# Performance work log

Hardware: AMD Instinct MI355X
Metric: run time of the kernel (lower is better)

The kernel has to match this reference:

```python
import jax, jax.numpy as jnp
import numpy as np

B, N, D_MODEL = 16, 65536, 512
NBUCKETS = 11
BN_EPS = 1e-5
LN_EPS = 1e-5


def setup_inputs() -> dict:
    key = jax.random.key(0)
    ks = jax.random.split(key, 12)
    def w(k, shape, fan_in):
        return jax.random.normal(k, shape, jnp.float32) * (1.0 / np.sqrt(fan_in))
    return {
        "x": jax.random.normal(ks[0], (B, N, 3), jnp.float32),
        "w1": w(ks[1], (3, 64), 3),   "b1": jnp.zeros((64,), jnp.float32),
        "g1": jnp.ones((64,), jnp.float32),  "be1": jnp.zeros((64,), jnp.float32),
        "w2": w(ks[2], (64, 128), 64), "b2": jnp.zeros((128,), jnp.float32),
        "g2": jnp.ones((128,), jnp.float32), "be2": jnp.zeros((128,), jnp.float32),
        "w3": w(ks[3], (128, 256), 128), "b3": jnp.zeros((256,), jnp.float32),
        "g3": jnp.ones((256,), jnp.float32), "be3": jnp.zeros((256,), jnp.float32),
        "wp": w(ks[4], (518, D_MODEL), 518), "bp": jnp.zeros((D_MODEL,), jnp.float32),
        "g_ln": jnp.ones((D_MODEL,), jnp.float32), "b_ln": jnp.zeros((D_MODEL,), jnp.float32),
    }


def _bn(h, g, b):
    # BatchNorm1d in training mode: biased variance over the flattened batch axis
    m = jnp.mean(h, axis=0)
    v = jnp.mean((h - m) ** 2, axis=0)
    return (h - m) * jax.lax.rsqrt(v + BN_EPS) * g + b


def reference(x, w1, b1, g1, be1, w2, b2, g2, be2, w3, b3, g3, be3, wp, bp, g_ln, b_ln):
    Bb, Nn, _ = x.shape
    x_flat = x.reshape(Bb * Nn, 3)
    h = jax.nn.relu(_bn(x_flat @ w1 + b1, g1, be1))
    h = jax.nn.relu(_bn(h @ w2 + b2, g2, be2))
    h = jax.nn.relu(_bn(h @ w3 + b3, g3, be3))
    feat = h.reshape(Bb, Nn, 256)

    # y-bucket histogram means of (x, z) coordinates, vectorized via segment_sum
    y = x[:, :, 1]
    y_min = jnp.min(y, axis=1, keepdims=True)
    y_max = jnp.max(y, axis=1, keepdims=True)
    y_norm = (y - y_min) / (y_max - y_min + 1e-6)
    buckets = jnp.clip((y_norm * 10).astype(jnp.int32), 0, NBUCKETS - 1)  # (B,N) in [0,10]
    seg = (jnp.arange(Bb, dtype=jnp.int32)[:, None] * NBUCKETS + buckets).reshape(-1)
    nseg = Bb * NBUCKETS
    sx = jax.ops.segment_sum(x[:, :, 0].reshape(-1), seg, num_segments=nseg)
    sz = jax.ops.segment_sum(x[:, :, 2].reshape(-1), seg, num_segments=nseg)
    cnt = jax.ops.segment_sum(jnp.ones((Bb * Nn,), jnp.float32), seg, num_segments=nseg)
    denom = jnp.maximum(cnt, 1.0)
    cx = (sx / denom).reshape(Bb, NBUCKETS)
    cz = (sz / denom).reshape(Bb, NBUCKETS)
    x_centers = jnp.take_along_axis(cx, buckets, axis=1)  # (B,N)
    z_centers = jnp.take_along_axis(cz, buckets, axis=1)

    dx = x[:, :, 0] - x_centers
    dz = x[:, :, 2] - z_centers
    theta = jnp.arctan2(dz, dx)
    r = jnp.sqrt(dx ** 2 + dz ** 2)
    spatial = jnp.stack([jnp.sin(theta), jnp.cos(theta), r], axis=-1)  # (B,N,3)

    feat = jnp.concatenate([feat, spatial], axis=-1)  # (B,N,259)
    feat_max = jnp.max(feat, axis=1)
    feat_avg = jnp.mean(feat, axis=1)
    feat_cat = jnp.concatenate([feat_max, feat_avg], axis=1)  # (B,518)

    out = feat_cat @ wp + bp
    mu = jnp.mean(out, axis=-1, keepdims=True)
    var = jnp.mean((out - mu) ** 2, axis=-1, keepdims=True)
    return (out - mu) * jax.lax.rsqrt(var + LN_EPS) * g_ln + b_ln
```

## Files before the change

### kernel.cpp

```cpp
#include <hip/hip_runtime.h>
#include <stdint.h>

#define B_    16
#define N_    65536
#define NPTS  (B_*N_)
#define NBK   11
#define NFEAT 259
#define NF    ((float)NPTS)

typedef float f32x4 __attribute__((ext_vector_type(4)));
typedef short s16x8 __attribute__((ext_vector_type(8)));
union frag_u { s16x8 v; unsigned u[4]; };
union x24_u  { float4 v4[6]; float f[24]; };

enum {
  OFF_YMINF = 16,
  OFF_YMAXF = 32,
  OFF_A1    = 64,
  OFF_C1    = 128,
  OFF_A2    = 192,
  OFF_C2    = 320,
  OFF_CX    = 448,
  OFF_CZ    = 624,
  OFF_A3    = 800,
  OFF_C3    = 1056,
  OFF_GC    = 2048,
  OFF_G1S   = 6144,
  OFF_H3C   = 6400,
  OFF_PSTR  = 16384,
  OFF_PBKT  = 24576,
  OFF_PSPA  = 43008,
  OFF_PG    = 49152,
  OFF_PGS   = 2146304,
  OFF_PH3   = 2179072,
  OFF_PPOOL = 2703360
};

__device__ __forceinline__ float wave_sum(float v){
  #pragma unroll
  for (int m=32;m>=1;m>>=1) v += __shfl_xor(v,m,64);
  return v;
}
__device__ __forceinline__ float wave_max(float v){
  #pragma unroll
  for (int m=32;m>=1;m>>=1) v = fmaxf(v,__shfl_xor(v,m,64));
  return v;
}
__device__ __forceinline__ float wave_min(float v){
  #pragma unroll
  for (int m=32;m>=1;m>>=1) v = fminf(v,__shfl_xor(v,m,64));
  return v;
}
__device__ __forceinline__ unsigned short bf16_bits(float f){
  unsigned u=__float_as_uint(f);
  u += 0x7FFFu + ((u>>16)&1u);
  return (unsigned short)(u>>16);
}
__device__ __forceinline__ unsigned cvt_pk_bf16(float lo, float hi){
  unsigned r;
  asm("v_cvt_pk_bf16_f32 %0, %1, %2" : "=v"(r) : "v"(lo), "v"(hi));
  return r;
}

__global__ __launch_bounds__(256) void k_stream0(const float* __restrict__ x,
                                                 float* __restrict__ ws){
  __shared__ float red[4][12];
  const int t=threadIdx.x, l=t&63, w=t>>6;
  const int bid=blockIdx.x;
  const float4* xv=(const float4*)(x + (size_t)bid*2048*3);
  float s0=0,s1=0,s2=0,q00=0,q01=0,q02=0,q11=0,q12=0,q22=0;
  float ymn=3.4e38f, ymx=-3.4e38f;
  #pragma unroll
  for (int i=0;i<2;i++){
    const int vi=(i*256+t)*3;
    const float4 a=xv[vi], b4=xv[vi+1], c=xv[vi+2];
    float X[4]={a.x,a.w,b4.z,c.y};
    float Y[4]={a.y,b4.x,b4.w,c.z};
    float Z[4]={a.z,b4.y,c.x,c.w};
    #pragma unroll
    for (int p=0;p<4;p++){
      s0+=X[p]; s1+=Y[p]; s2+=Z[p];
      q00=fmaf(X[p],X[p],q00); q01=fmaf(X[p],Y[p],q01); q02=fmaf(X[p],Z[p],q02);
      q11=fmaf(Y[p],Y[p],q11); q12=fmaf(Y[p],Z[p],q12); q22=fmaf(Z[p],Z[p],q22);
      ymn=fminf(ymn,Y[p]); ymx=fmaxf(ymx,Y[p]);
    }
  }
  s0=wave_sum(s0); s1=wave_sum(s1); s2=wave_sum(s2);
  q00=wave_sum(q00); q01=wave_sum(q01); q02=wave_sum(q02);
  q11=wave_sum(q11); q12=wave_sum(q12); q22=wave_sum(q22);
  ymn=wave_min(ymn); ymx=wave_max(ymx);
  if (l==0){
    red[w][0]=s0; red[w][1]=s1; red[w][2]=s2;
    red[w][3]=q00; red[w][4]=q01; red[w][5]=q02;
    red[w][6]=q11; red[w][7]=q12; red[w][8]=q22;
    red[w][9]=ymn; red[w][10]=ymx;
  }
  __syncthreads();
  if (t<11){
    const float v0=red[0][t],v1=red[1][t],v2=red[2][t],v3=red[3][t];
    float r;
    if (t==9)       r=fminf(fminf(v0,v1),fminf(v2,v3));
    else if (t==10) r=fmaxf(fmaxf(v0,v1),fmaxf(v2,v3));
    else            r=v0+v1+v2+v3;
    ws[OFF_PSTR+bid*16+t]=r;
  }
}

__global__ void k_finA(const float* __restrict__ w1, const float* __restrict__ b1,
                       const float* __restrict__ gm, const float* __restrict__ bt,
                       float* __restrict__ ws){
  __shared__ float sums[9];
  const int t=threadIdx.x;
  if (t<9){
    float s=0.f;
    #pragma unroll 8
    for (int blk=0;blk<512;blk++) s+=ws[OFF_PSTR+blk*16+t];
    sums[t]=s;
  }
  if (t>=32&&t<48){
    const int b=t-32; float m=3.4e38f;
    #pragma unroll 8
    for (int blk=0;blk<32;blk++) m=fminf(m,ws[OFF_PSTR+(b*32+blk)*16+9]);
    ws[OFF_YMINF+b]=m;
  }
  if (t>=48&&t<64){
    const int b=t-48; float m=-3.4e38f;
    #pragma unroll 8
    for (int blk=0;blk<32;blk++) m=fmaxf(m,ws[OFF_PSTR+(b*32+blk)*16+10]);
    ws[OFF_YMAXF+b]=m;
  }
  __syncthreads();
  if (t<64){
    const float i_n=1.f/NF;
    const float w0=w1[t], wa=w1[64+t], wb=w1[128+t];
    const float ms=(w0*sums[0]+wa*sums[1]+wb*sums[2])*i_n;
    const float es=(w0*w0*sums[3]+wa*wa*sums[6]+wb*wb*sums[8]
                   +2.f*(w0*wa*sums[4]+w0*wb*sums[5]+wa*wb*sums[7]))*i_n;
    const float var=es-ms*ms;
    const float a=gm[t]/sqrtf(var+1e-5f);
    ws[OFF_A1+t]=a; ws[OFF_C1+t]=bt[t]-(ms+b1[t])*a;
  }
}

__global__ __launch_bounds__(256) void k_bucket(const float* __restrict__ x,
                                                float* __restrict__ ws){
  __shared__ float red[4][12];
  const int t=threadIdx.x, l=t&63, w=t>>6;
  const int bid=blockIdx.x, b=bid>>5;
  const float ymn=ws[OFF_YMINF+b], ymx=ws[OFF_YMAXF+b];
  const float4* xv=(const float4*)(x + (size_t)bid*2048*3);
  float sxl[NBK], szl[NBK], cntl[NBK];
  #pragma unroll
  for (int k=0;k<NBK;k++){ sxl[k]=0.f; szl[k]=0.f; cntl[k]=0.f; }
  #pragma unroll
  for (int i=0;i<2;i++){
    const int vi=(i*256+t)*3;
    const float4 a=xv[vi], b4=xv[vi+1], c=xv[vi+2];
    float X[4]={a.x,a.w,b4.z,c.y};
    float Y[4]={a.y,b4.x,b4.w,c.z};
    float Z[4]={a.z,b4.y,c.x,c.w};
    #pragma unroll
    for (int p=0;p<4;p++){
      const float yn=(Y[p]-ymn)/(ymx-ymn+1e-6f);
      int bk=(int)(yn*10.f); bk = bk<0?0:(bk>10?10:bk);
      #pragma unroll
      for (int k=0;k<NBK;k++){
        const bool m=(bk==k);
        sxl[k]+= m?X[p]:0.f; szl[k]+= m?Z[p]:0.f; cntl[k]+= m?1.f:0.f;
      }
    }
  }
  #pragma unroll
  for (int k=0;k<NBK;k++){
    const float s=wave_sum(sxl[k]);
    if (l==0) red[w][k]=s;
  }
  __syncthreads();
  if (t<NBK) ws[OFF_PBKT+bid*36+t]=red[0][t]+red[1][t]+red[2][t]+red[3][t];
  __syncthreads();
  #pragma unroll
  for (int k=0;k<NBK;k++){
    const float z=wave_sum(szl[k]);
    if (l==0) red[w][k]=z;
  }
  __syncthreads();
  if (t<NBK) ws[OFF_PBKT+bid*36+11+t]=red[0][t]+red[1][t]+red[2][t]+red[3][t];
  __syncthreads();
  #pragma unroll
  for (int k=0;k<NBK;k++){
    const float c=wave_sum(cntl[k]);
    if (l==0) red[w][k]=c;
  }
  __syncthreads();
  if (t<NBK) ws[OFF_PBKT+bid*36+22+t]=red[0][t]+red[1][t]+red[2][t]+red[3][t];
}

__global__ __launch_bounds__(256) void k_spatial(const float* __restrict__ x,
                                                 float* __restrict__ ws){
  __shared__ float red[4][8];
  const int t=threadIdx.x, l=t&63, w=t>>6;
  const int bid=blockIdx.x, b=bid>>5;
  const float ymn=ws[OFF_YMINF+b], ymx=ws[OFF_YMAXF+b];
  const float4* xv=(const float4*)(x + (size_t)bid*2048*3);
  float mx[3]={-3.4e38f,-3.4e38f,-3.4e38f}, sm[3]={0.f,0.f,0.f};
  #pragma unroll
  for (int i=0;i<2;i++){
    const int vi=(i*256+t)*3;
    const float4 a=xv[vi], b4=xv[vi+1], c=xv[vi+2];
    float X[4]={a.x,a.w,b4.z,c.y};
    float Y[4]={a.y,b4.x,b4.w,c.z};
    float Z[4]={a.z,b4.y,c.x,c.w};
    #pragma unroll
    for (int p=0;p<4;p++){
      const float yn=(Y[p]-ymn)/(ymx-ymn+1e-6f);
      int bk=(int)(yn*10.f); bk = bk<0?0:(bk>10?10:bk);
      const float dx=X[p]-ws[OFF_CX+b*NBK+bk];
      const float dz=Z[p]-ws[OFF_CZ+b*NBK+bk];
      const float r=sqrtf(fmaf(dx,dx,dz*dz));
      const float sn=(r>0.f)?(dz/r):0.f;
      const float cs=(r>0.f)?(dx/r):1.f;
      mx[0]=fmaxf(mx[0],sn); sm[0]+=sn;
      mx[1]=fmaxf(mx[1],cs); sm[1]+=cs;
      mx[2]=fmaxf(mx[2],r);  sm[2]+=r;
    }
  }
  #pragma unroll
  for (int q=0;q<3;q++){
    const float m=wave_max(mx[q]);
    const float s=wave_sum(sm[q]);
    if (l==0){ red[w][q]=m; red[w][4+q]=s; }
  }
  __syncthreads();
  if (t<3)        ws[OFF_PSPA+bid*8+t]  =fmaxf(fmaxf(red[0][t],red[1][t]),fmaxf(red[2][t],red[3][t]));
  else if (t>=4&&t<7){
    const int q=t-4;
    ws[OFF_PSPA+bid*8+4+q]=red[0][4+q]+red[1][4+q]+red[2][4+q]+red[3][4+q];
  }
}

__global__ __launch_bounds__(512,2) void k_gram(
    const float* __restrict__ x,
    const float* __restrict__ w1, const float* __restrict__ b1,
    float* __restrict__ ws)
{
  const int t=threadIdx.x, w=t>>6, l=t&63, lg=l>>4, lr=l&15;
  const int bid=blockIdx.x;
  const int ti=w>>1, tj0=(w&1)*2, tj1=tj0+1;
  const float* A1=ws+OFF_A1; const float* C1=ws+OFF_C1;
  float wA[4], wB0[4], wB1[4];
  {
    const int fA=16*ti+lr;  const float aA=A1[fA];
    wA[0]=w1[fA]*aA;  wA[1]=w1[64+fA]*aA;  wA[2]=w1[128+fA]*aA;  wA[3]=b1[fA]*aA+C1[fA];
    const int f0=16*tj0+lr; const float a0=A1[f0];
    wB0[0]=w1[f0]*a0; wB0[1]=w1[64+f0]*a0; wB0[2]=w1[128+f0]*a0; wB0[3]=b1[f0]*a0+C1[f0];
    const int f1=16*tj1+lr; const float a1=A1[f1];
    wB1[0]=w1[f1]*a1; wB1[1]=w1[64+f1]*a1; wB1[2]=w1[128+f1]*a1; wB1[3]=b1[f1]*a1+C1[f1];
  }
  f32x4 acc0={0.f,0.f,0.f,0.f}, acc1={0.f,0.f,0.f,0.f};
  float s1=0.f;
  const float* xb = x + (size_t)bid*2048*3;
  #pragma unroll 1
  for (int step=0; step<64; ++step){
    x24_u xa;
    const float4* xp=(const float4*)(xb + (step*32+8*lg)*3);
    #pragma unroll
    for (int i=0;i<6;i++) xa.v4[i]=xp[i];
    float gA[8],gB0[8],gB1[8];
    #pragma unroll
    for (int j=0;j<8;j++){
      const float X=xa.f[3*j], Y=xa.f[3*j+1], Z=xa.f[3*j+2];
      gA[j] =fmaxf(fmaf(X,wA[0], fmaf(Y,wA[1], fmaf(Z,wA[2], wA[3]))),0.f);
      gB0[j]=fmaxf(fmaf(X,wB0[0],fmaf(Y,wB0[1],fmaf(Z,wB0[2],wB0[3]))),0.f);
      gB1[j]=fmaxf(fmaf(X,wB1[0],fmaf(Y,wB1[1],fmaf(Z,wB1[2],wB1[3]))),0.f);
    }
    frag_u fA,f0,f1;
    #pragma unroll
    for (int m=0;m<4;m++){
      fA.u[m]=cvt_pk_bf16(gA[2*m],gA[2*m+1]);
      f0.u[m]=cvt_pk_bf16(gB0[2*m],gB0[2*m+1]);
      f1.u[m]=cvt_pk_bf16(gB1[2*m],gB1[2*m+1]);
    }
    acc0=__builtin_amdgcn_mfma_f32_16x16x32_bf16(fA.v,f0.v,acc0,0,0,0);
    acc1=__builtin_amdgcn_mfma_f32_16x16x32_bf16(fA.v,f1.v,acc1,0,0,0);
    if (!(w&1)){
      #pragma unroll
      for (int j=0;j<8;j++) s1+=gA[j];
    }
  }
  #pragma unroll
  for (int q=0;q<4;q++){
    ws[OFF_PG + (size_t)((16*ti+4*lg+q)*64 + 16*tj0+lr)*512 + bid]=acc0[q];
    ws[OFF_PG + (size_t)((16*ti+4*lg+q)*64 + 16*tj1+lr)*512 + bid]=acc1[q];
  }
  if (!(w&1)){
    s1+=__shfl_xor(s1,16); s1+=__shfl_xor(s1,32);
    if (l<16) ws[OFF_PGS + (16*ti+lr)*512 + bid]=s1;
  }
}

__global__ __launch_bounds__(256) void k_redG(float* __restrict__ ws){
  __shared__ float red[256];
  const int t=threadIdx.x, blk=blockIdx.x;
  if (blk<64){
    const int e=blk*64+(t>>2), q=t&3;
    float s=0.f;
    const float* p=ws+OFF_PG+(size_t)e*512+q*128;
    #pragma unroll 8
    for (int i=0;i<128;i++) s+=p[i];
    red[t]=s; __syncthreads();
    if (q==0) ws[OFF_GC+e]=red[t]+red[t+1]+red[t+2]+red[t+3];
  } else {
    const int f=t>>2, q=t&3;
    float s=0.f;
    const float* p=ws+OFF_PGS+(size_t)f*512+q*128;
    #pragma unroll 8
    for (int i=0;i<128;i++) s+=p[i];
    red[t]=s; __syncthreads();
    if (q==0) ws[OFF_G1S+f]=red[t]+red[t+1]+red[t+2]+red[t+3];
  }
}

__global__ __launch_bounds__(256) void k_finB2(
    const float* __restrict__ w2, const float* __restrict__ b2,
    const float* __restrict__ gm, const float* __restrict__ bt,
    float* __restrict__ ws){
  __shared__ float red[256];
  __shared__ float red2[64];
  const int t=threadIdx.x, j=blockIdx.x;
  if (j<128){
    float acc=0.f;
    #pragma unroll
    for (int p=0;p<16;p++){
      const int idx=p*256+t;
      const int r=idx>>6, c=idx&63;
      acc += w2[r*128+j]*ws[OFF_GC+r*64+c]*w2[c*128+j];
    }
    red[t]=acc;
    if (t<64) red2[t]=w2[t*128+j]*ws[OFF_G1S+t];
    __syncthreads();
    for (int s=128;s>0;s>>=1){ if (t<s) red[t]+=red[t+s]; __syncthreads(); }
    if (t<32) red2[t]+=red2[t+32];
    __syncthreads();
    if (t==0){
      float sw=0.f;
      #pragma unroll
      for (int i=0;i<32;i++) sw+=red2[i];
      const float i_n=1.f/NF;
      const float bj=b2[j];
      const float m=sw*i_n+bj;
      const float e2=(red[0]+2.f*bj*sw)*i_n+bj*bj;
      const float var=e2-m*m;
      const float a=gm[j]/sqrtf(var+1e-5f);
      ws[OFF_A2+j]=a; ws[OFF_C2+j]=bt[j]-m*a;
    }
  } else {
    if (t<176){
      const int b=t/NBK, k=t-b*NBK;
      float sx=0.f, sz=0.f, cn=0.f;
      #pragma unroll 8
      for (int blk=0;blk<32;blk++){
        const int p=OFF_PBKT+(b*32+blk)*36;
        sx+=ws[p+k]; sz+=ws[p+11+k]; cn+=ws[p+22+k];
      }
      const float d=fmaxf(cn,1.f);
      ws[OFF_CX+t]=sx/d; ws[OFF_CZ+t]=sz/d;
    }
  }
}

template<int MODE>
__global__ __launch_bounds__(512) void k_mlp(
    const float* __restrict__ x,
    const float* __restrict__ w1, const float* __restrict__ b1,
    const float* __restrict__ w2, const float* __restrict__ b2,
    const float* __restrict__ w3, const float* __restrict__ b3,
    float* __restrict__ ws)
{
  __shared__ float xs[2048*3];
  __shared__ short g2t[2*128*136];
  const int t=threadIdx.x, w=t>>6, l=t&63, lg=l>>4, lr=l&15;
  const int bid=blockIdx.x;
  const int ptg=w&1, fgrp=w>>1;
  char* g2base=(char*)g2t;

  {
    const float4* xp=(const float4*)(x + (size_t)bid*2048*3);
    float4* xd=(float4*)xs;
    #pragma unroll
    for (int i=0;i<3;i++) xd[i*512+t]=xp[i*512+t];
  }

  const float* A1=ws+OFF_A1; const float* C1=ws+OFF_C1;
  float w1f[2][3][8], b1f[2][8];
  #pragma unroll
  for (int kt=0;kt<2;kt++)
    #pragma unroll
    for (int i=0;i<8;i++){
      const int f=kt*32+8*lg+i; const float a=A1[f];
      w1f[kt][0][i]=w1[f]*a; w1f[kt][1][i]=w1[64+f]*a; w1f[kt][2][i]=w1[128+f]*a;
      b1f[kt][i]=b1[f]*a+C1[f];
    }

  s16x8 w2f[2][2]; float b2i[2][4];
  #pragma unroll
  for (int j=0;j<2;j++){
    const int col2=(2*fgrp+j)*16+lr;
    const float sc2=ws[OFF_A2+col2];
    #pragma unroll
    for (int kt=0;kt<2;kt++)
      #pragma unroll
      for (int i=0;i<8;i++)
        w2f[j][kt][i]=(short)bf16_bits(w2[(kt*32+8*lg+i)*128+col2]*sc2);
    #pragma unroll
    for (int r=0;r<4;r++){
      const int f2=(2*fgrp+j)*16+4*lg+r;
      b2i[j][r]=ws[OFF_A2+f2]*b2[f2]+ws[OFF_C2+f2];
    }
  }

  s16x8 w3f[4][4]; float b3i[4][4];
  #pragma unroll
  for (int j=0;j<4;j++){
    const int col3=(4*fgrp+j)*16+lr;
    const float sc3=(MODE==1)?1.f:ws[OFF_A3+col3];
    #pragma unroll
    for (int kt=0;kt<4;kt++)
      #pragma unroll
      for (int i=0;i<8;i++)
        w3f[j][kt][i]=(short)bf16_bits(w3[(kt*32+8*lg+i)*256+col3]*sc3);
    #pragma unroll
    for (int r=0;r<4;r++){
      const int f3=(4*fgrp+j)*16+4*lg+r;
      b3i[j][r]=(MODE==1)? b3[f3] : (ws[OFF_A3+f3]*b3[f3]+ws[OFF_C3+f3]);
    }
  }

  float aS[4][4], aQ[4][4];
  #pragma unroll
  for (int j=0;j<4;j++)
    #pragma unroll
    for (int r=0;r<4;r++){ aS[j][r]=(MODE==2)?-3.4e38f:0.f; aQ[j][r]=0.f; }

  __syncthreads();

  int cur=0;
  #pragma unroll 1
  for (int it=0; it<16; ++it){
    char* g2cur=g2base + cur*(128*272);
    #pragma unroll
    for (int pt=0;pt<4;pt++){
      const int row=ptg*64+pt*16+lr;
      const int pidx=it*128+row;
      const float x0=xs[pidx*3+0], x1v=xs[pidx*3+1], x2=xs[pidx*3+2];
      frag_u bf[2];
      #pragma unroll
      for (int kt=0;kt<2;kt++){
        float h[8];
        #pragma unroll
        for (int i=0;i<8;i++){
          float v=b1f[kt][i];
          v=fmaf(x0,w1f[kt][0][i],v); v=fmaf(x1v,w1f[kt][1][i],v); v=fmaf(x2,w1f[kt][2][i],v);
          h[i]=fmaxf(v,0.f);
        }
        #pragma unroll
        for (int m=0;m<4;m++) bf[kt].u[m]=cvt_pk_bf16(h[2*m],h[2*m+1]);
      }
      #pragma unroll
      for (int j=0;j<2;j++){
        f32x4 acc={b2i[j][0],b2i[j][1],b2i[j][2],b2i[j][3]};
        acc=__builtin_amdgcn_mfma_f32_16x16x32_bf16(w2f[j][0],bf[0].v,acc,0,0,0);
        acc=__builtin_amdgcn_mfma_f32_16x16x32_bf16(w2f[j][1],bf[1].v,acc,0,0,0);
        const unsigned lo=cvt_pk_bf16(fmaxf(acc[0],0.f),fmaxf(acc[1],0.f));
        const unsigned hi=cvt_pk_bf16(fmaxf(acc[2],0.f),fmaxf(acc[3],0.f));
        *(uint2*)(g2cur + row*272 + fgrp*64 + j*32 + lg*8)=make_uint2(lo,hi);
      }
    }
    __syncthreads();
    #pragma unroll 1
    for (int pt=0;pt<4;pt++){
      const int row=ptg*64+pt*16+lr;
      const char* rp=g2cur + row*272;
      s16x8 bfr0=*(const s16x8*)(rp + lg*16);
      s16x8 bfr1=*(const s16x8*)(rp + 64 + lg*16);
      s16x8 bfr2=*(const s16x8*)(rp + 128 + lg*16);
      s16x8 bfr3=*(const s16x8*)(rp + 192 + lg*16);
      #pragma unroll
      for (int j=0;j<4;j++){
        f32x4 a3={b3i[j][0],b3i[j][1],b3i[j][2],b3i[j][3]};
        a3=__builtin_amdgcn_mfma_f32_16x16x32_bf16(w3f[j][0],bfr0,a3,0,0,0);
        a3=__builtin_amdgcn_mfma_f32_16x16x32_bf16(w3f[j][1],bfr1,a3,0,0,0);
        a3=__builtin_amdgcn_mfma_f32_16x16x32_bf16(w3f[j][2],bfr2,a3,0,0,0);
        a3=__builtin_amdgcn_mfma_f32_16x16x32_bf16(w3f[j][3],bfr3,a3,0,0,0);
        #pragma unroll
        for (int r=0;r<4;r++){
          if (MODE==1){
            const float h=a3[r]; aS[j][r]+=h; aQ[j][r]=fmaf(h,h,aQ[j][r]);
          } else {
            const float g=fmaxf(a3[r],0.f);
            aS[j][r]=fmaxf(aS[j][r],g); aQ[j][r]+=g;
          }
        }
      }
    }
    cur^=1;
  }

  const int slot=bid*2+ptg;
  #pragma unroll
  for (int j=0;j<4;j++)
    #pragma unroll
    for (int r=0;r<4;r++){
      const int f3=(4*fgrp+j)*16+4*lg+r;
      if (MODE==1){
        float s=aS[j][r], q=aQ[j][r];
        #pragma unroll
        for (int m=1;m<16;m<<=1){ s+=__shfl_xor(s,m); q+=__shfl_xor(q,m); }
        if (lr==0){
          ws[OFF_PH3 + (size_t)f3*1024 + slot]=s;
          ws[OFF_PH3 + (size_t)(256+f3)*1024 + slot]=q;
        }
      } else {
        float mxv=aS[j][r], s=aQ[j][r];
        #pragma unroll
        for (int m=1;m<16;m<<=1){ mxv=fmaxf(mxv,__shfl_xor(mxv,m)); s+=__shfl_xor(s,m); }
        if (lr==0){
          const int b=bid>>5, chunk=bid&31;
          ws[OFF_PPOOL + (size_t)b*512*64 + (size_t)f3*64 + chunk*2+ptg]=mxv;
          ws[OFF_PPOOL + (size_t)b*512*64 + (size_t)(256+f3)*64 + chunk*2+ptg]=s;
        }
      }
    }
}

__global__ __launch_bounds__(256) void k_redH3(float* __restrict__ ws){
  __shared__ float red[256];
  const int t=threadIdx.x, blk=blockIdx.x;
  const int col=blk*16+(t>>4), part=t&15;
  float s=0.f;
  const float* p=ws+OFF_PH3+(size_t)col*1024+part*64;
  #pragma unroll 8
  for (int i=0;i<64;i++) s+=p[i];
  red[t]=s; __syncthreads();
  if (part==0){
    float r=0.f;
    #pragma unroll
    for (int i=0;i<16;i++) r+=red[(t&~15)+i];
    ws[OFF_H3C+col]=r;
  }
}

__global__ void k_finC(const float* __restrict__ gm, const float* __restrict__ bt,
                       float* __restrict__ ws){
  const int t=threadIdx.x;
  if (t<256){
    const float i_n=1.f/NF;
    const float m=ws[OFF_H3C+t]*i_n;
    const float v=ws[OFF_H3C+256+t]*i_n-m*m;
    const float a=gm[t]/sqrtf(v+1e-5f);
    ws[OFF_A3+t]=a; ws[OFF_C3+t]=bt[t]-m*a;
  }
}

__global__ __launch_bounds__(256) void k_final(
    const float* __restrict__ wp, const float* __restrict__ bp,
    const float* __restrict__ gln, const float* __restrict__ bln,
    float* __restrict__ out, const float* __restrict__ ws)
{
  __shared__ float feat[518];
  __shared__ float red[256];
  const int b=blockIdx.x, t=threadIdx.x;
  {
    float fm=-3.4e38f, fs=0.f;
    const float* pm=ws+OFF_PPOOL+(size_t)b*512*64+(size_t)t*64;
    const float* psu=ws+OFF_PPOOL+(size_t)b*512*64+(size_t)(256+t)*64;
    #pragma unroll 8
    for (int s=0;s<64;s++){ fm=fmaxf(fm,pm[s]); fs+=psu[s]; }
    feat[t]=fm; feat[NFEAT+t]=fs*(1.f/65536.f);
  }
  if (t<3){
    float fm=-3.4e38f, fs=0.f;
    #pragma unroll 4
    for (int blk=0;blk<32;blk++){
      const int p=OFF_PSPA+(b*32+blk)*8;
      fm=fmaxf(fm,ws[p+t]);
      fs+=ws[p+4+t];
    }
    feat[256+t]=fm; feat[NFEAT+256+t]=fs*(1.f/65536.f);
  }
  __syncthreads();
  float o0=bp[t], o1=bp[t+256];
  #pragma unroll 4
  for (int i=0;i<518;i++){
    const float f=feat[i];
    o0=fmaf(f, wp[i*512+t],     o0);
    o1=fmaf(f, wp[i*512+t+256], o1);
  }
  red[t]=o0+o1; __syncthreads();
  for (int s=128;s>0;s>>=1){ if (t<s) red[t]+=red[t+s]; __syncthreads(); }
  const float mu=red[0]*(1.f/512.f);
  __syncthreads();
  const float d0=o0-mu, d1=o1-mu;
  red[t]=d0*d0+d1*d1; __syncthreads();
  for (int s=128;s>0;s>>=1){ if (t<s) red[t]+=red[t+s]; __syncthreads(); }
  const float var=red[0]*(1.f/512.f);
  const float rs=1.f/sqrtf(var+1e-5f);
  out[b*512+t]     = d0*rs*gln[t]    +bln[t];
  out[b*512+t+256] = d1*rs*gln[t+256]+bln[t+256];
}

extern "C" void kernel_launch(void* const* d_in, const int* in_sizes, int n_in,
                              void* d_out, int out_size, void* d_ws, size_t ws_size,
                              hipStream_t stream)
{
  const float* x  =(const float*)d_in[0];
  const float* w1 =(const float*)d_in[1];
  const float* b1 =(const float*)d_in[2];
  const float* gm1=(const float*)d_in[3];
  const float* be1=(const float*)d_in[4];
  const float* w2 =(const float*)d_in[5];
  const float* b2 =(const float*)d_in[6];
  const float* gm2=(const float*)d_in[7];
  const float* be2=(const float*)d_in[8];
  const float* w3 =(const float*)d_in[9];
  const float* b3 =(const float*)d_in[10];
  const float* gm3=(const float*)d_in[11];
  const float* be3=(const float*)d_in[12];
  const float* wp =(const float*)d_in[13];
  const float* bp =(const float*)d_in[14];
  const float* gln=(const float*)d_in[15];
  const float* bln=(const float*)d_in[16];
  float* ws=(float*)d_ws;
  float* out=(float*)d_out;

  k_stream0<<<dim3(512),dim3(256),0,stream>>>(x,ws);
  k_finA   <<<dim3(1),  dim3(256),0,stream>>>(w1,b1,gm1,be1,ws);
  k_bucket <<<dim3(512),dim3(256),0,stream>>>(x,ws);
  k_gram   <<<dim3(512),dim3(512),0,stream>>>(x,w1,b1,ws);
  k_redG   <<<dim3(65), dim3(256),0,stream>>>(ws);
  k_finB2  <<<dim3(129),dim3(256),0,stream>>>(w2,b2,gm2,be2,ws);
  k_spatial<<<dim3(512),dim3(256),0,stream>>>(x,ws);
  k_mlp<1> <<<dim3(512),dim3(512),0,stream>>>(x,w1,b1,w2,b2,w3,b3,ws);
  k_redH3  <<<dim3(32), dim3(256),0,stream>>>(ws);
  k_finC   <<<dim3(1),  dim3(256),0,stream>>>(gm3,be3,ws);
  k_mlp<2> <<<dim3(512),dim3(512),0,stream>>>(x,w1,b1,w2,b2,w3,b3,ws);
  k_final  <<<dim3(16), dim3(256),0,stream>>>(wp,bp,gln,bln,out,ws);
}
```

Measured before the change: 477.1 us.

## Restructure MLP kernel for two blocks per CU with shared layer-1 tile

```diff
diff --git a/kernel.cpp b/kernel.cpp
--- a/kernel.cpp
+++ b/kernel.cpp
@@ -33,7 +33,7 @@
   OFF_PG    = 49152,
   OFF_PGS   = 2146304,
   OFF_PH3   = 2179072,
-  OFF_PPOOL = 2703360
+  OFF_PPOOL = 3227648
 };
 
 __device__ __forceinline__ float wave_sum(float v){
@@ -369,39 +369,32 @@
 }
 
 template<int MODE>
-__global__ __launch_bounds__(512) void k_mlp(
+__global__ __launch_bounds__(512,2) void k_mlp(
     const float* __restrict__ x,
     const float* __restrict__ w1, const float* __restrict__ b1,
     const float* __restrict__ w2, const float* __restrict__ b2,
     const float* __restrict__ w3, const float* __restrict__ b3,
     float* __restrict__ ws)
 {
-  __shared__ float xs[2048*3];
-  __shared__ short g2t[2*128*136];
+  __shared__ short g1t[128*72];
+  __shared__ short g2t[128*136];
   const int t=threadIdx.x, w=t>>6, l=t&63, lg=l>>4, lr=l&15;
-  const int bid=blockIdx.x;
+  const int bid=blockIdx.x, b=bid>>6, chunk=bid&63;
   const int ptg=w&1, fgrp=w>>1;
-  char* g2base=(char*)g2t;
-
-  {
-    const float4* xp=(const float4*)(x + (size_t)bid*2048*3);
-    float4* xd=(float4*)xs;
-    #pragma unroll
-    for (int i=0;i<3;i++) xd[i*512+t]=xp[i*512+t];
-  }
-
-  const float* A1=ws+OFF_A1; const float* C1=ws+OFF_C1;
-  float w1f[2][3][8], b1f[2][8];
-  #pragma unroll
-  for (int kt=0;kt<2;kt++)
-    #pragma unroll
-    for (int i=0;i<8;i++){
-      const int f=kt*32+8*lg+i; const float a=A1[f];
-      w1f[kt][0][i]=w1[f]*a; w1f[kt][1][i]=w1[64+f]*a; w1f[kt][2][i]=w1[128+f]*a;
-      b1f[kt][i]=b1[f]*a+C1[f];
-    }
-
-  s16x8 w2f[2][2]; float b2i[2][4];
+  char* g1c=(char*)g1t; char* g2c=(char*)g2t;
+
+  const int fg=l&7, pj=(l>>3)&7;
+  const float* a1=ws+OFF_A1; const float* c1=ws+OFF_C1;
+  float w1f[3][8], b1f[8];
+  #pragma unroll
+  for (int i=0;i<8;i++){
+    const int f=8*fg+i; const float a=a1[f];
+    #pragma unroll
+    for (int q=0;q<3;q++) w1f[q][i]=w1[q*64+f]*a;
+    b1f[i]=b1[f]*a+c1[f];
+  }
+
+  s16x8 w2f[2][2]; float b2v[2][4];
   #pragma unroll
   for (int j=0;j<2;j++){
     const int col2=(2*fgrp+j)*16+lr;
@@ -414,11 +407,11 @@
     #pragma unroll
     for (int r=0;r<4;r++){
       const int f2=(2*fgrp+j)*16+4*lg+r;
-      b2i[j][r]=ws[OFF_A2+f2]*b2[f2]+ws[OFF_C2+f2];
-    }
-  }
-
-  s16x8 w3f[4][4]; float b3i[4][4];
+      b2v[j][r]=ws[OFF_A2+f2]*b2[f2]+ws[OFF_C2+f2];
+    }
+  }
+
+  s16x8 w3f[4][4]; float b3v[4][4];
   #pragma unroll
   for (int j=0;j<4;j++){
     const int col3=(4*fgrp+j)*16+lr;
@@ -431,7 +424,7 @@
     #pragma unroll
     for (int r=0;r<4;r++){
       const int f3=(4*fgrp+j)*16+4*lg+r;
-      b3i[j][r]=(MODE==1)? b3[f3] : (ws[OFF_A3+f3]*b3[f3]+ws[OFF_C3+f3]);
+      b3v[j][r]=(MODE==1)? b3[f3] : (ws[OFF_A3+f3]*b3[f3]+ws[OFF_C3+f3]);
     }
   }
 
@@ -441,56 +434,68 @@
     #pragma unroll
     for (int r=0;r<4;r++){ aS[j][r]=(MODE==2)?-3.4e38f:0.f; aQ[j][r]=0.f; }
 
-  __syncthreads();
-
-  int cur=0;
+  const int base=b*N_+chunk*1024;
+  const int ptl=16*w+2*pj;
+
+  float c0[3], c1v[3], n0[3], n1[3];
+  {
+    const float* xp=&x[(size_t)(base+ptl)*3];
+    #pragma unroll
+    for (int q=0;q<3;q++){ c0[q]=xp[q]; c1v[q]=xp[3+q]; }
+  }
+
   #pragma unroll 1
-  for (int it=0; it<16; ++it){
-    char* g2cur=g2base + cur*(128*272);
+  for (int it=0; it<8; ++it){
+    #pragma unroll
+    for (int s=0;s<2;s++){
+      const float x0=s?c1v[0]:c0[0], x1v=s?c1v[1]:c0[1], x2=s?c1v[2]:c0[2];
+      unsigned pk[4];
+      #pragma unroll
+      for (int i=0;i<4;i++){
+        float v0=b1f[2*i], v1=b1f[2*i+1];
+        v0=fmaf(x0,w1f[0][2*i],v0);  v1=fmaf(x0,w1f[0][2*i+1],v1);
+        v0=fmaf(x1v,w1f[1][2*i],v0); v1=fmaf(x1v,w1f[1][2*i+1],v1);
+        v0=fmaf(x2,w1f[2][2*i],v0);  v1=fmaf(x2,w1f[2][2*i+1],v1);
+        pk[i]=cvt_pk_bf16(fmaxf(v0,0.f),fmaxf(v1,0.f));
+      }
+      *(int4*)(g1c + (ptl+s)*144 + fg*16) = make_int4(pk[0],pk[1],pk[2],pk[3]);
+    }
+    if (it<7){
+      const float* xp=&x[(size_t)(base+(it+1)*128+ptl)*3];
+      #pragma unroll
+      for (int q=0;q<3;q++){ n0[q]=xp[q]; n1[q]=xp[3+q]; }
+    }
+    __syncthreads();
     #pragma unroll
     for (int pt=0;pt<4;pt++){
       const int row=ptg*64+pt*16+lr;
-      const int pidx=it*128+row;
-      const float x0=xs[pidx*3+0], x1v=xs[pidx*3+1], x2=xs[pidx*3+2];
-      frag_u bf[2];
-      #pragma unroll
-      for (int kt=0;kt<2;kt++){
-        float h[8];
-        #pragma unroll
-        for (int i=0;i<8;i++){
-          float v=b1f[kt][i];
-          v=fmaf(x0,w1f[kt][0][i],v); v=fmaf(x1v,w1f[kt][1][i],v); v=fmaf(x2,w1f[kt][2][i],v);
-          h[i]=fmaxf(v,0.f);
-        }
-        #pragma unroll
-        for (int m=0;m<4;m++) bf[kt].u[m]=cvt_pk_bf16(h[2*m],h[2*m+1]);
-      }
+      const s16x8 bf0=*(const s16x8*)(g1c + row*144 + lg*16);
+      const s16x8 bf1=*(const s16x8*)(g1c + row*144 + 64 + lg*16);
       #pragma unroll
       for (int j=0;j<2;j++){
-        f32x4 acc={b2i[j][0],b2i[j][1],b2i[j][2],b2i[j][3]};
-        acc=__builtin_amdgcn_mfma_f32_16x16x32_bf16(w2f[j][0],bf[0].v,acc,0,0,0);
-        acc=__builtin_amdgcn_mfma_f32_16x16x32_bf16(w2f[j][1],bf[1].v,acc,0,0,0);
+        f32x4 acc={b2v[j][0],b2v[j][1],b2v[j][2],b2v[j][3]};
+        acc=__builtin_amdgcn_mfma_f32_16x16x32_bf16(w2f[j][0],bf0,acc,0,0,0);
+        acc=__builtin_amdgcn_mfma_f32_16x16x32_bf16(w2f[j][1],bf1,acc,0,0,0);
         const unsigned lo=cvt_pk_bf16(fmaxf(acc[0],0.f),fmaxf(acc[1],0.f));
         const unsigned hi=cvt_pk_bf16(fmaxf(acc[2],0.f),fmaxf(acc[3],0.f));
-        *(uint2*)(g2cur + row*272 + fgrp*64 + j*32 + lg*8)=make_uint2(lo,hi);
+        *(uint2*)(g2c + row*272 + fgrp*64 + j*32 + lg*8) = make_uint2(lo,hi);
       }
     }
     __syncthreads();
     #pragma unroll 1
     for (int pt=0;pt<4;pt++){
       const int row=ptg*64+pt*16+lr;
-      const char* rp=g2cur + row*272;
-      s16x8 bfr0=*(const s16x8*)(rp + lg*16);
-      s16x8 bfr1=*(const s16x8*)(rp + 64 + lg*16);
-      s16x8 bfr2=*(const s16x8*)(rp + 128 + lg*16);
-      s16x8 bfr3=*(const s16x8*)(rp + 192 + lg*16);
+      const s16x8 bf0=*(const s16x8*)(g2c + row*272 + lg*16);
+      const s16x8 bf1=*(const s16x8*)(g2c + row*272 + 64 + lg*16);
+      const s16x8 bf2=*(const s16x8*)(g2c + row*272 + 128 + lg*16);
+      const s16x8 bf3=*(const s16x8*)(g2c + row*272 + 192 + lg*16);
       #pragma unroll
       for (int j=0;j<4;j++){
-        f32x4 a3={b3i[j][0],b3i[j][1],b3i[j][2],b3i[j][3]};
-        a3=__builtin_amdgcn_mfma_f32_16x16x32_bf16(w3f[j][0],bfr0,a3,0,0,0);
-        a3=__builtin_amdgcn_mfma_f32_16x16x32_bf16(w3f[j][1],bfr1,a3,0,0,0);
-        a3=__builtin_amdgcn_mfma_f32_16x16x32_bf16(w3f[j][2],bfr2,a3,0,0,0);
-        a3=__builtin_amdgcn_mfma_f32_16x16x32_bf16(w3f[j][3],bfr3,a3,0,0,0);
+        f32x4 a3={b3v[j][0],b3v[j][1],b3v[j][2],b3v[j][3]};
+        a3=__builtin_amdgcn_mfma_f32_16x16x32_bf16(w3f[j][0],bf0,a3,0,0,0);
+        a3=__builtin_amdgcn_mfma_f32_16x16x32_bf16(w3f[j][1],bf1,a3,0,0,0);
+        a3=__builtin_amdgcn_mfma_f32_16x16x32_bf16(w3f[j][2],bf2,a3,0,0,0);
+        a3=__builtin_amdgcn_mfma_f32_16x16x32_bf16(w3f[j][3],bf3,a3,0,0,0);
         #pragma unroll
         for (int r=0;r<4;r++){
           if (MODE==1){
@@ -502,10 +507,10 @@
         }
       }
     }
-    cur^=1;
-  }
-
-  const int slot=bid*2+ptg;
+    #pragma unroll
+    for (int q=0;q<3;q++){ c0[q]=n0[q]; c1v[q]=n1[q]; }
+  }
+
   #pragma unroll
   for (int j=0;j<4;j++)
     #pragma unroll
@@ -516,17 +521,18 @@
         #pragma unroll
         for (int m=1;m<16;m<<=1){ s+=__shfl_xor(s,m); q+=__shfl_xor(q,m); }
         if (lr==0){
-          ws[OFF_PH3 + (size_t)f3*1024 + slot]=s;
-          ws[OFF_PH3 + (size_t)(256+f3)*1024 + slot]=q;
+          const int slot=bid*2+ptg;
+          ws[OFF_PH3 + (size_t)f3*2048 + slot]=s;
+          ws[OFF_PH3 + (size_t)(256+f3)*2048 + slot]=q;
         }
       } else {
         float mxv=aS[j][r], s=aQ[j][r];
         #pragma unroll
         for (int m=1;m<16;m<<=1){ mxv=fmaxf(mxv,__shfl_xor(mxv,m)); s+=__shfl_xor(s,m); }
         if (lr==0){
-          const int b=bid>>5, chunk=bid&31;
-          ws[OFF_PPOOL + (size_t)b*512*64 + (size_t)f3*64 + chunk*2+ptg]=mxv;
-          ws[OFF_PPOOL + (size_t)b*512*64 + (size_t)(256+f3)*64 + chunk*2+ptg]=s;
+          const int slot=chunk*2+ptg;
+          ws[OFF_PPOOL + (size_t)b*512*128 + (size_t)f3*128 + slot]=mxv;
+          ws[OFF_PPOOL + (size_t)b*512*128 + (size_t)(256+f3)*128 + slot]=s;
         }
       }
     }
@@ -537,9 +543,9 @@
   const int t=threadIdx.x, blk=blockIdx.x;
   const int col=blk*16+(t>>4), part=t&15;
   float s=0.f;
-  const float* p=ws+OFF_PH3+(size_t)col*1024+part*64;
+  const float* p=ws+OFF_PH3+(size_t)col*2048+part*128;
   #pragma unroll 8
-  for (int i=0;i<64;i++) s+=p[i];
+  for (int i=0;i<128;i++) s+=p[i];
   red[t]=s; __syncthreads();
   if (part==0){
     float r=0.f;
@@ -571,10 +577,10 @@
   const int b=blockIdx.x, t=threadIdx.x;
   {
     float fm=-3.4e38f, fs=0.f;
-    const float* pm=ws+OFF_PPOOL+(size_t)b*512*64+(size_t)t*64;
-    const float* psu=ws+OFF_PPOOL+(size_t)b*512*64+(size_t)(256+t)*64;
+    const float* pm =ws+OFF_PPOOL+(size_t)b*512*128+(size_t)t*128;
+    const float* psu=ws+OFF_PPOOL+(size_t)b*512*128+(size_t)(256+t)*128;
     #pragma unroll 8
-    for (int s=0;s<64;s++){ fm=fmaxf(fm,pm[s]); fs+=psu[s]; }
+    for (int s=0;s<128;s++){ fm=fmaxf(fm,pm[s]); fs+=psu[s]; }
     feat[t]=fm; feat[NFEAT+t]=fs*(1.f/65536.f);
   }
   if (t<3){
@@ -632,16 +638,16 @@
   float* ws=(float*)d_ws;
   float* out=(float*)d_out;
 
-  k_stream0<<<dim3(512),dim3(256),0,stream>>>(x,ws);
-  k_finA   <<<dim3(1),  dim3(256),0,stream>>>(w1,b1,gm1,be1,ws);
-  k_bucket <<<dim3(512),dim3(256),0,stream>>>(x,ws);
-  k_gram   <<<dim3(512),dim3(512),0,stream>>>(x,w1,b1,ws);
-  k_redG   <<<dim3(65), dim3(256),0,stream>>>(ws);
-  k_finB2  <<<dim3(129),dim3(256),0,stream>>>(w2,b2,gm2,be2,ws);
-  k_spatial<<<dim3(512),dim3(256),0,stream>>>(x,ws);
-  k_mlp<1> <<<dim3(512),dim3(512),0,stream>>>(x,w1,b1,w2,b2,w3,b3,ws);
-  k_redH3  <<<dim3(32), dim3(256),0,stream>>>(ws);
-  k_finC   <<<dim3(1),  dim3(256),0,stream>>>(gm3,be3,ws);
-  k_mlp<2> <<<dim3(512),dim3(512),0,stream>>>(x,w1,b1,w2,b2,w3,b3,ws);
-  k_final  <<<dim3(16), dim3(256),0,stream>>>(wp,bp,gln,bln,out,ws);
-}
+  k_stream0<<<dim3(512), dim3(256),0,stream>>>(x,ws);
+  k_finA   <<<dim3(1),   dim3(256),0,stream>>>(w1,b1,gm1,be1,ws);
+  k_bucket <<<dim3(512), dim3(256),0,stream>>>(x,ws);
+  k_gram   <<<dim3(512), dim3(512),0,stream>>>(x,w1,b1,ws);
+  k_redG   <<<dim3(65),  dim3(256),0,stream>>>(ws);
+  k_finB2  <<<dim3(129), dim3(256),0,stream>>>(w2,b2,gm2,be2,ws);
+  k_spatial<<<dim3(512), dim3(256),0,stream>>>(x,ws);
+  k_mlp<1> <<<dim3(1024),dim3(512),0,stream>>>(x,w1,b1,w2,b2,w3,b3,ws);
+  k_redH3  <<<dim3(32),  dim3(256),0,stream>>>(ws);
+  k_finC   <<<dim3(1),   dim3(256),0,stream>>>(gm3,be3,ws);
+  k_mlp<2> <<<dim3(1024),dim3(512),0,stream>>>(x,w1,b1,w2,b2,w3,b3,ws);
+  k_final  <<<dim3(16),  dim3(256),0,stream>>>(wp,bp,gln,bln,out,ws);
+}
```

Measured after the change: 446.9 us. 6.3% less time.
